# Performance work log

Hardware: AMD Instinct MI355X
Metric: run time of the kernel (lower is better)

The kernel has to match this reference:

```python
import jax, jax.numpy as jnp
import numpy as np

BS, L, D, H, NL, ITEM_NUM = 128, 64, 512, 8, 2, 100000
NEG_INF = -10000.0


def _ln(x):
    m = jnp.mean(x, axis=-1, keepdims=True)
    v = jnp.var(x, axis=-1, keepdims=True)
    return (x - m) * jax.lax.rsqrt(v + 1e-5)


def _user_encoder(input_embs, log_mask, pos_emb, qkv_w, out_w, ffn_w1, ffn_w2):
    # SASRec-style causal transformer encoder (post-LN blocks)
    B, S, d = input_embs.shape
    dh = d // H
    x = _ln(input_embs + pos_emb[None, :, :])
    pad = (log_mask != 0)                                  # [B,S]
    causal = jnp.tril(jnp.ones((S, S), dtype=bool))
    attn_ok = causal[None, :, :] & pad[:, None, :]         # [B,S,S]
    bias = jnp.where(attn_ok, 0.0, NEG_INF)[:, None, :, :]  # [B,1,S,S]
    for l in range(NL):
        qkv = x @ qkv_w[l]                                 # [B,S,3d]
        q, k, v = jnp.split(qkv, 3, axis=-1)
        q = q.reshape(B, S, H, dh).transpose(0, 2, 1, 3)
        k = k.reshape(B, S, H, dh).transpose(0, 2, 1, 3)
        v = v.reshape(B, S, H, dh).transpose(0, 2, 1, 3)
        scores = jnp.einsum('bhqd,bhkd->bhqk', q, k) / jnp.sqrt(jnp.asarray(dh, x.dtype)) + bias
        attn = jax.nn.softmax(scores, axis=-1)
        o = jnp.einsum('bhqk,bhkd->bhqd', attn, v).transpose(0, 2, 1, 3).reshape(B, S, d)
        x = _ln(x + o @ out_w[l])
        h = jax.nn.gelu(x @ ffn_w1[l])
        x = _ln(x + h @ ffn_w2[l])
    return x


def setup_inputs() -> dict:
    key = jax.random.key(0)
    ks = jax.random.split(key, 9)
    sample_items_id = jax.random.randint(ks[0], (BS, L + 1), 0, ITEM_NUM + 1)
    log_mask = jax.random.randint(ks[1], (BS, L), 0, 2).astype(jnp.float32)
    emb_table = (jax.random.normal(ks[2], (ITEM_NUM + 1, D), jnp.float32) * 0.02).at[0].set(0.0)
    pos_emb = jax.random.normal(ks[3], (L, D), jnp.float32) * 0.02
    qkv_w = jax.random.normal(ks[4], (NL, D, 3 * D), jnp.float32) * (D ** -0.5)
    out_w = jax.random.normal(ks[5], (NL, D, D), jnp.float32) * (D ** -0.5)
    ffn_w1 = jax.random.normal(ks[6], (NL, D, 4 * D), jnp.float32) * (D ** -0.5)
    ffn_w2 = jax.random.normal(ks[7], (NL, 4 * D, D), jnp.float32) * ((4 * D) ** -0.5)
    pop_prob = jax.random.uniform(ks[8], (ITEM_NUM + 1,), jnp.float32, 1e-6, 1.0)
    return dict(sample_items_id=sample_items_id, log_mask=log_mask, emb_table=emb_table,
                pos_emb=pos_emb, qkv_w=qkv_w, out_w=out_w, ffn_w1=ffn_w1, ffn_w2=ffn_w2,
                pop_prob=pop_prob)


def reference(sample_items_id, log_mask, emb_table, pos_emb, qkv_w, out_w, ffn_w1, ffn_w2, pop_prob):
    bs, l = log_mask.shape
    N = bs * (l + 1)
    items_flat = sample_items_id.reshape(-1)                        # [N]
    debias = jnp.log(pop_prob[items_flat])                          # [N]
    score_embs = emb_table[items_flat]                              # [N, D]
    input_embs = score_embs.reshape(bs, l + 1, -1)
    prec = _user_encoder(input_embs[:, :-1, :], log_mask, pos_emb, qkv_w, out_w, ffn_w1, ffn_w2)
    prec = prec.reshape(bs * l, -1)                                 # [bs*L, D]
    logits = prec @ score_embs.T - debias[None, :]                  # [bs*L, N]
    # padding-column mask (concat(log_mask, ones) == 0)
    pad_cols = jnp.concatenate([log_mask, jnp.ones((bs, 1), log_mask.dtype)], axis=1).reshape(-1) == 0
    logits = jnp.where(pad_cols[None, :], NEG_INF, logits)
    logits = logits.reshape(bs, l, N)
    # in-batch dedup mask: column k masked for batch i if item k appears in batch i's items
    id_list = sample_items_id.reshape(bs, l + 1)
    member = (items_flat[None, :, None] == id_list[:, None, :]).any(-1)   # [bs, N]
    target_col = jnp.arange(bs)[:, None] * (l + 1) + jnp.arange(1, l + 1)[None, :]  # [bs, L]
    is_target = jnp.arange(N)[None, None, :] == target_col[:, :, None]    # [bs, L, N]
    dedup = member[:, None, :] & ~is_target
    logits = jnp.where(dedup, NEG_INF, logits).reshape(bs * l, N)
    labels = target_col.reshape(-1)                                 # [bs*L]
    logp = jax.nn.log_softmax(logits, axis=-1)
    nll = -jnp.take_along_axis(logp, labels[:, None], axis=1)[:, 0]
    valid = (log_mask.reshape(-1) != 0).astype(logits.dtype)
    return (nll * valid).sum() / valid.sum()
```

## Files before the change

kernel.cpp:

```cpp
#include <hip/hip_runtime.h>
#include <hip/hip_bf16.h>
#include <cstdint>
#include <cstddef>

#define NEG_INF -10000.0f

constexpr int BSZ  = 128;
constexpr int SEQ  = 64;
constexpr int DIM  = 512;
constexpr int HEADS = 8;
constexpr int NLAYER = 2;
constexpr int NCOL = BSZ * (SEQ + 1);
constexpr int NCOLP = 8448;
constexpr int NROW = BSZ * SEQ;
constexpr int NSTRIP = NCOLP / 64;
constexpr float CMAX = 40.0f;
constexpr float LOG2E = 1.4426950408889634f;

typedef __attribute__((ext_vector_type(8))) short bf16x8;
typedef __attribute__((ext_vector_type(4))) float f32x4;

__device__ __forceinline__ void async_copy16(const void* g, void* l) {
    __builtin_amdgcn_global_load_lds(
        (const __attribute__((address_space(1))) void*)g,
        (__attribute__((address_space(3))) void*)l, 16, 0, 0);
}

__device__ __forceinline__ float b2f(uint16_t u) {
    return __builtin_bit_cast(float, (uint32_t)u << 16);
}
__device__ __forceinline__ uint16_t f2b(float f) {
    __hip_bfloat16 h = __float2bfloat16(f);
    return __builtin_bit_cast(uint16_t, h);
}

__device__ __forceinline__ float fexp2(float x) {
    float r; asm("v_exp_f32 %0, %1" : "=v"(r) : "v"(x)); return r;
}

__device__ __forceinline__ float gelu_f(float v) {
    float u = 0.7978845608028654f * (v + 0.044715f * v * v * v);
    float t2 = fexp2(u * (2.0f * LOG2E));
    float th = 1.0f - 2.0f * __builtin_amdgcn_rcpf(t2 + 1.0f);
    return 0.5f * v * (1.0f + th);
}

__device__ __forceinline__ void swizzle_rc(int id, int& ry, int& cx) {
    ry = (id & 7) * 8 + ((id >> 3) & 7);
    cx = id >> 6;
}

#define BAR() __builtin_amdgcn_s_barrier()
#define LGKM0() asm volatile("s_waitcnt lgkmcnt(0)" ::: "memory")
#define VMCNT(n) asm volatile("s_waitcnt vmcnt(" #n ")" ::: "memory")

__global__ __launch_bounds__(256) void gather_posln_kernel(
    const int* __restrict__ ids, const float* __restrict__ table,
    const float* __restrict__ pop, const float* __restrict__ pos,
    __hip_bfloat16* __restrict__ sebf, float* __restrict__ debias,
    float* __restrict__ deb2, __hip_bfloat16* __restrict__ xb) {
    const int w = threadIdx.x >> 6, lane = threadIdx.x & 63;
    const int k = blockIdx.x * 4 + w;
    const int b = k / 65, s = k - b * 65;
    const int id = ids[k];
    const float* src = table + (size_t)id * DIM + lane * 8;
    float4 u0 = *(const float4*)src;
    float4 u1 = *(const float4*)(src + 4);
    float v[8] = {u0.x, u0.y, u0.z, u0.w, u1.x, u1.y, u1.z, u1.w};
    bf16x8 se;
    #pragma unroll
    for (int j = 0; j < 8; j++) se[j] = (short)f2b(v[j]);
    *(bf16x8*)((uint16_t*)sebf + (size_t)k * DIM + lane * 8) = se;
    if (lane == 0) {
        const float lp = logf(pop[id]);
        debias[k] = lp;
        deb2[k] = (lp + CMAX) * LOG2E;
    }
    if (s < 64) {
        const float* pp = pos + (size_t)s * DIM + lane * 8;
        float4 p0 = *(const float4*)pp;
        float4 p1 = *(const float4*)(pp + 4);
        float t[8] = {v[0] + p0.x, v[1] + p0.y, v[2] + p0.z, v[3] + p0.w,
                      v[4] + p1.x, v[5] + p1.y, v[6] + p1.z, v[7] + p1.w};
        float sum = 0.f, sq = 0.f;
        #pragma unroll
        for (int j = 0; j < 8; j++) { sum += t[j]; sq += t[j] * t[j]; }
        #pragma unroll
        for (int off = 32; off > 0; off >>= 1) {
            sum += __shfl_xor(sum, off, 64);
            sq  += __shfl_xor(sq,  off, 64);
        }
        const float mean = sum * (1.0f / 512.0f);
        const float var  = sq * (1.0f / 512.0f) - mean * mean;
        const float rs = rsqrtf(var + 1e-5f);
        bf16x8 o;
        #pragma unroll
        for (int j = 0; j < 8; j++) o[j] = (short)f2b((t[j] - mean) * rs);
        *(bf16x8*)((uint16_t*)xb + (size_t)(b * 64 + s) * DIM + lane * 8) = o;
    }
}

__global__ __launch_bounds__(256) void mask_kernel(
    const int* __restrict__ ids, const float* __restrict__ log_mask,
    uint8_t* __restrict__ colmask, uint8_t* __restrict__ padcol) {
    const int bi = blockIdx.x >> 3, seg = blockIdx.x & 7;
    __shared__ int sid[65];
    if (threadIdx.x < 65) sid[threadIdx.x] = ids[bi * 65 + threadIdx.x];
    __syncthreads();
    const int kend = (seg + 1) * (NCOLP / 8);
    for (int k = seg * (NCOLP / 8) + threadIdx.x; k < kend; k += 256) {
        uint8_t cmv, pcv;
        if (k < NCOL) {
            const int id = ids[k];
            bool mem = false;
            #pragma unroll
            for (int j = 0; j < 65; j++) mem |= (sid[j] == id);
            const int i2 = k / 65, jj = k - i2 * 65;
            const bool pc = (jj < 64) && (log_mask[i2 * 64 + jj] == 0.0f);
            cmv = (mem || pc) ? 1 : 0;
            pcv = pc ? 1 : 0;
        } else { cmv = 1; pcv = 1; }
        colmask[(size_t)bi * NCOLP + k] = cmv;
        if (bi == 0) padcol[k] = pcv;
    }
}

__global__ __launch_bounds__(256) void transpose_bf16_kernel(
    const float* __restrict__ W, __hip_bfloat16* __restrict__ WT, int K, int N) {
    __shared__ float tile[32][33];
    const size_t loff = (size_t)blockIdx.z * K * N;
    const int nt = blockIdx.x * 32, kt = blockIdx.y * 32;
    const int c = threadIdx.x & 31, r = threadIdx.x >> 5;
    #pragma unroll
    for (int p = 0; p < 4; p++)
        tile[p * 8 + r][c] = W[loff + (size_t)(kt + p * 8 + r) * N + nt + c];
    __syncthreads();
    #pragma unroll
    for (int p = 0; p < 4; p++)
        WT[loff + (size_t)(nt + p * 8 + r) * K + kt + c] = __float2bfloat16(tile[c][p * 8 + r]);
}

template<bool SCALED>
__global__ __launch_bounds__(256) void resid_ln_kernel(
    __hip_bfloat16* __restrict__ xb, const __hip_bfloat16* __restrict__ y,
    __hip_bfloat16* __restrict__ xs) {
    const int w = threadIdx.x >> 6, lane = threadIdx.x & 63;
    const int row = blockIdx.x * 4 + w;
    uint16_t* xp = (uint16_t*)xb + (size_t)row * DIM + lane * 8;
    const uint16_t* yp = (const uint16_t*)y + (size_t)row * DIM + lane * 8;
    bf16x8 xv = *(const bf16x8*)xp;
    bf16x8 yv = *(const bf16x8*)yp;
    float t[8];
    float sum = 0.f, sq = 0.f;
    #pragma unroll
    for (int j = 0; j < 8; j++) {
        t[j] = b2f((uint16_t)xv[j]) + b2f((uint16_t)yv[j]);
        sum += t[j]; sq += t[j] * t[j];
    }
    #pragma unroll
    for (int off = 32; off > 0; off >>= 1) {
        sum += __shfl_xor(sum, off, 64);
        sq  += __shfl_xor(sq,  off, 64);
    }
    const float mean = sum * (1.0f / 512.0f);
    const float var  = sq * (1.0f / 512.0f) - mean * mean;
    const float rs = rsqrtf(var + 1e-5f);
    bf16x8 o;
    #pragma unroll
    for (int j = 0; j < 8; j++) o[j] = (short)f2b((t[j] - mean) * rs);
    *(bf16x8*)xp = o;
    if (SCALED) {
        bf16x8 os;
        #pragma unroll
        for (int j = 0; j < 8; j++) os[j] = (short)f2b((t[j] - mean) * rs * LOG2E);
        *(bf16x8*)((uint16_t*)xs + (size_t)row * DIM + lane * 8) = os;
    }
}

template<int TN, bool GELU>
__global__ __launch_bounds__(256) void gemm_bt_kernel(
    const __hip_bfloat16* __restrict__ A, const __hip_bfloat16* __restrict__ Bt,
    __hip_bfloat16* __restrict__ C, int N, int K) {
    __shared__ uint16_t As[2][128][32];
    __shared__ uint16_t Bs[2][TN][32];
    const int tid = threadIdx.x, w = tid >> 6, lane = tid & 63;
    const int quad = lane >> 4, l15 = lane & 15;
    constexpr int AI = (TN == 128) ? 4 : 2;
    const int wr = (TN == 128) ? (w >> 1) : w;
    const int wc = (TN == 128) ? (w & 1) : 0;
    const int rowbase = wr * (AI * 16);
    int ry, cx;
    swizzle_rc(blockIdx.x, ry, cx);
    const int row0 = ry * 128, col0 = cx * TN;
    const uint16_t* Ag = (const uint16_t*)A;
    const uint16_t* Bg = (const uint16_t*)Bt;
    const int sr = lane >> 2, sc = (lane & 3) * 8;
    f32x4 acc[AI][4];
    #pragma unroll
    for (int i = 0; i < AI; i++)
        #pragma unroll
        for (int j = 0; j < 4; j++) acc[i][j] = {0.f, 0.f, 0.f, 0.f};

    for (int k0 = 0; k0 < K; k0 += 64) {
        #pragma unroll
        for (int h = 0; h < 2; h++) {
            #pragma unroll
            for (int i = 0; i < 2; i++) {
                const int rb = w * 32 + i * 16;
                async_copy16(Ag + (size_t)(row0 + rb + sr) * K + k0 + h * 32 + sc, &As[h][rb][0]);
            }
            if (TN == 128) {
                #pragma unroll
                for (int i = 0; i < 2; i++) {
                    const int rb = w * 32 + i * 16;
                    async_copy16(Bg + (size_t)(col0 + rb + sr) * K + k0 + h * 32 + sc, &Bs[h][rb][0]);
                }
            } else {
                const int rb = w * 16;
                async_copy16(Bg + (size_t)(col0 + rb + sr) * K + k0 + h * 32 + sc, &Bs[h][rb][0]);
            }
        }
        __syncthreads();
        #pragma unroll
        for (int h = 0; h < 2; h++) {
            bf16x8 af[AI], bfr[4];
            #pragma unroll
            for (int i = 0; i < AI; i++)
                af[i] = *(const bf16x8*)&As[h][rowbase + i * 16 + l15][quad * 8];
            #pragma unroll
            for (int j = 0; j < 4; j++)
                bfr[j] = *(const bf16x8*)&Bs[h][wc * 64 + j * 16 + l15][quad * 8];
            #pragma unroll
            for (int i = 0; i < AI; i++)
                #pragma unroll
                for (int j = 0; j < 4; j++)
                    acc[i][j] = __builtin_amdgcn_mfma_f32_16x16x32_bf16(af[i], bfr[j], acc[i][j], 0, 0, 0);
        }
        __syncthreads();
    }
    #pragma unroll
    for (int i = 0; i < AI; i++) {
        #pragma unroll
        for (int r = 0; r < 4; r++) {
            const int row = row0 + rowbase + i * 16 + quad * 4 + r;
            #pragma unroll
            for (int j = 0; j < 4; j++) {
                const int col = col0 + wc * 64 + j * 16 + l15;
                float v = acc[i][j][r];
                if (GELU) v = gelu_f(v);
                C[(size_t)row * N + col] = __float2bfloat16(v);
            }
        }
    }
}

__global__ __launch_bounds__(256) void attn_mfma_kernel(
    const __hip_bfloat16* __restrict__ qkv, const float* __restrict__ log_mask,
    __hip_bfloat16* __restrict__ obuf) {
    constexpr int QS = 72;
    constexpr int VS32 = 36;
    __shared__ uint16_t Qs[64 * QS];
    __shared__ uint16_t Ks_[64 * QS];
    __shared__ uint16_t Ps[64 * QS];
    __shared__ uint32_t Vt32[64 * VS32];
    __shared__ float mask_s[64];
    const int b = blockIdx.x >> 3, h = blockIdx.x & 7;
    const int tid = threadIdx.x, w = tid >> 6, lane = tid & 63;
    const int quad = lane >> 4, l15 = lane & 15;
    const uint16_t* qg = (const uint16_t*)qkv;

    if (tid < 64) mask_s[tid] = log_mask[b * 64 + tid];
    #pragma unroll
    for (int it = 0; it < 2; it++) {
        const int idx = it * 256 + tid;
        const int s = idx >> 3, c = (idx & 7) * 8;
        const size_t gbase = (size_t)(b * 64 + s) * 1536 + h * 64 + c;
        *(bf16x8*)&Qs[s * QS + c]  = *(const bf16x8*)&qg[gbase];
        *(bf16x8*)&Ks_[s * QS + c] = *(const bf16x8*)&qg[gbase + 512];
    }
    {
        const int sp = tid >> 3;
        const int c = (tid & 7) * 8;
        const size_t gbase = (size_t)(b * 64 + sp * 2) * 1536 + 1024 + h * 64 + c;
        bf16x8 v0 = *(const bf16x8*)&qg[gbase];
        bf16x8 v1 = *(const bf16x8*)&qg[gbase + 1536];
        #pragma unroll
        for (int jj = 0; jj < 8; jj++)
            Vt32[(c + jj) * VS32 + sp] =
                (uint32_t)(uint16_t)v0[jj] | ((uint32_t)(uint16_t)v1[jj] << 16);
    }
    __syncthreads();

    f32x4 sacc[4];
    #pragma unroll
    for (int j = 0; j < 4; j++) sacc[j] = {0.f, 0.f, 0.f, 0.f};
    #pragma unroll
    for (int k0 = 0; k0 < 2; k0++) {
        bf16x8 aq = *(const bf16x8*)&Qs[(w * 16 + l15) * QS + k0 * 32 + quad * 8];
        #pragma unroll
        for (int j = 0; j < 4; j++) {
            bf16x8 bk = *(const bf16x8*)&Ks_[(j * 16 + l15) * QS + k0 * 32 + quad * 8];
            sacc[j] = __builtin_amdgcn_mfma_f32_16x16x32_bf16(aq, bk, sacc[j], 0, 0, 0);
        }
    }
    #pragma unroll
    for (int r = 0; r < 4; r++) {
        const int q = w * 16 + quad * 4 + r;
        float vals[4];
        float vmax = -3.0e38f;
        #pragma unroll
        for (int j = 0; j < 4; j++) {
            const int col = j * 16 + l15;
            const bool ok = (col <= q) && (mask_s[col] != 0.0f);
            float v = sacc[j][r] * 0.125f + (ok ? 0.0f : NEG_INF);
            vals[j] = v;
            vmax = fmaxf(vmax, v);
        }
        #pragma unroll
        for (int off = 1; off < 16; off <<= 1) vmax = fmaxf(vmax, __shfl_xor(vmax, off, 64));
        float e[4], s = 0.f;
        #pragma unroll
        for (int j = 0; j < 4; j++) { e[j] = fexp2((vals[j] - vmax) * LOG2E); s += e[j]; }
        #pragma unroll
        for (int off = 1; off < 16; off <<= 1) s += __shfl_xor(s, off, 64);
        const float inv = 1.0f / s;
        #pragma unroll
        for (int j = 0; j < 4; j++)
            Ps[q * QS + j * 16 + l15] = f2b(e[j] * inv);
    }
    __syncthreads();

    f32x4 oacc[4];
    #pragma unroll
    for (int j = 0; j < 4; j++) oacc[j] = {0.f, 0.f, 0.f, 0.f};
    #pragma unroll
    for (int k0 = 0; k0 < 2; k0++) {
        bf16x8 ap = *(const bf16x8*)&Ps[(w * 16 + l15) * QS + k0 * 32 + quad * 8];
        #pragma unroll
        for (int j = 0; j < 4; j++) {
            bf16x8 bv = *(const bf16x8*)&Vt32[(j * 16 + l15) * VS32 + k0 * 16 + quad * 4];
            oacc[j] = __builtin_amdgcn_mfma_f32_16x16x32_bf16(ap, bv, oacc[j], 0, 0, 0);
        }
    }
    #pragma unroll
    for (int r = 0; r < 4; r++) {
        const int q = w * 16 + quad * 4 + r;
        #pragma unroll
        for (int j = 0; j < 4; j++) {
            const int d = j * 16 + l15;
            obuf[(size_t)(b * 64 + q) * 512 + h * 64 + d] = __float2bfloat16(oacc[j][r]);
        }
    }
}

__global__ __launch_bounds__(512) void gemm256_logits_kernel(
    const __hip_bfloat16* __restrict__ A, const __hip_bfloat16* __restrict__ Bt,
    int N, int K,
    const float* __restrict__ deb2, const uint8_t* __restrict__ colmask,
    float* __restrict__ partials) {
    __shared__ uint16_t SA[2][2][128 * 64];
    __shared__ uint16_t SB[2][2][128 * 64];
    __shared__ float dc_s[256];
    __shared__ uint8_t cm_s[4][256];

    const int tid = threadIdx.x;
    const int w = tid >> 6, lane = tid & 63;
    const int quad = lane >> 4, l15 = lane & 15;
    const int wr = w >> 2, wc = w & 3;

    const int nwg = gridDim.x;
    const int xid = (blockIdx.x & 7) * (nwg >> 3) + (blockIdx.x >> 3);
    const int ry = xid & 31, cx = xid >> 5;
    const int row0 = ry * 256, col0 = cx * 256;

    const uint16_t* Ag = (const uint16_t*)A;
    const uint16_t* Bg = (const uint16_t*)Bt;

    if (tid < 256) dc_s[tid] = deb2[col0 + tid];
    #pragma unroll
    for (int j = 0; j < 2; j++) {
        const int e = j * 512 + tid;
        cm_s[e >> 8][e & 255] =
            colmask[(size_t)((row0 >> 6) + (e >> 8)) * NCOLP + col0 + (e & 255)];
    }

    const int tb0 = w << 6, tb1 = 512 + (w << 6);
    const uint16_t* gA[2][2];
    const uint16_t* gB[2][2];
    #pragma unroll
    for (int j = 0; j < 2; j++) {
        const int t = j * 512 + (w << 6) + lane;
        const int r = t >> 3;
        const int s = (t & 7) ^ (r & 7);
        #pragma unroll
        for (int h = 0; h < 2; h++) {
            gA[h][j] = Ag + (size_t)(row0 + h * 128 + r) * K + s * 8;
            gB[h][j] = Bg + (size_t)(col0 + h * 128 + r) * K + s * 8;
        }
    }

    #define STAGE_A(tile, half, k0) do { \
        async_copy16(gA[half][0] + (k0), &SA[tile][half][tb0 * 8]); \
        async_copy16(gA[half][1] + (k0), &SA[tile][half][tb1 * 8]); } while (0)
    #define STAGE_B(tile, half, k0) do { \
        async_copy16(gB[half][0] + (k0), &SB[tile][half][tb0 * 8]); \
        async_copy16(gB[half][1] + (k0), &SB[tile][half][tb1 * 8]); } while (0)

    auto fragA = [&](int tile, int m, int kk) -> bf16x8 {
        return *(const bf16x8*)&SA[tile][wr]
            [((m * 16 + l15) << 6) + ((((kk << 2) + quad) ^ (l15 & 7)) << 3)];
    };
    auto fragB = [&](int tile, int n, int kk) -> bf16x8 {
        return *(const bf16x8*)&SB[tile][wc >> 1]
            [(((wc & 1) * 64 + n * 16 + l15) << 6) + ((((kk << 2) + quad) ^ (l15 & 7)) << 3)];
    };

    f32x4 acc[8][4];
    #pragma unroll
    for (int m = 0; m < 8; m++)
        #pragma unroll
        for (int n = 0; n < 4; n++) acc[m][n] = {0.f, 0.f, 0.f, 0.f};

    STAGE_A(0, 0, 0); STAGE_A(0, 1, 0);
    STAGE_B(0, 0, 0); STAGE_B(0, 1, 0);
    STAGE_A(1, 0, 64); STAGE_B(1, 0, 64);
    VMCNT(4);
    BAR();

    const int niters = K >> 7;
    bf16x8 af[4][2], bA[2][2], bB[2][2];
    for (int it = 0; it < niters; ++it) {
        const bool st = (it + 1 < niters);
        const int kc = it << 7;
        const int kn = kc + 128;

        #pragma unroll
        for (int m = 0; m < 4; m++) { af[m][0] = fragA(0, m, 0); af[m][1] = fragA(0, m, 1); }
        #pragma unroll
        for (int n = 0; n < 2; n++) { bA[n][0] = fragB(0, n, 0); bA[n][1] = fragB(0, n, 1); }
        STAGE_A(1, 1, kc + 64);
        BAR(); LGKM0();
        __builtin_amdgcn_s_setprio(1);
        #pragma unroll
        for (int m = 0; m < 4; m++)
            #pragma unroll
            for (int n = 0; n < 2; n++) {
                acc[m][n] = __builtin_amdgcn_mfma_f32_16x16x32_bf16(af[m][0], bA[n][0], acc[m][n], 0, 0, 0);
                acc[m][n] = __builtin_amdgcn_mfma_f32_16x16x32_bf16(af[m][1], bA[n][1], acc[m][n], 0, 0, 0);
            }
        __builtin_amdgcn_s_setprio(0);
        BAR();

        #pragma unroll
        for (int n = 0; n < 2; n++) { bB[n][0] = fragB(0, n + 2, 0); bB[n][1] = fragB(0, n + 2, 1); }
        STAGE_B(1, 1, kc + 64);
        BAR(); LGKM0();
        __builtin_amdgcn_s_setprio(1);
        #pragma unroll
        for (int m = 0; m < 4; m++)
            #pragma unroll
            for (int n = 0; n < 2; n++) {
                acc[m][n + 2] = __builtin_amdgcn_mfma_f32_16x16x32_bf16(af[m][0], bB[n][0], acc[m][n + 2], 0, 0, 0);
                acc[m][n + 2] = __builtin_amdgcn_mfma_f32_16x16x32_bf16(af[m][1], bB[n][1], acc[m][n + 2], 0, 0, 0);
            }
        __builtin_amdgcn_s_setprio(0);
        BAR();

        #pragma unroll
        for (int m = 0; m < 4; m++) { af[m][0] = fragA(0, m + 4, 0); af[m][1] = fragA(0, m + 4, 1); }
        if (st) STAGE_B(0, 0, kn);
        BAR(); LGKM0();
        __builtin_amdgcn_s_setprio(1);
        #pragma unroll
        for (int m = 0; m < 4; m++)
            #pragma unroll
            for (int n = 0; n < 2; n++) {
                acc[m + 4][n + 2] = __builtin_amdgcn_mfma_f32_16x16x32_bf16(af[m][0], bB[n][0], acc[m + 4][n + 2], 0, 0, 0);
                acc[m + 4][n + 2] = __builtin_amdgcn_mfma_f32_16x16x32_bf16(af[m][1], bB[n][1], acc[m + 4][n + 2], 0, 0, 0);
            }
        __builtin_amdgcn_s_setprio(0);
        BAR();

        if (st) STAGE_A(0, 0, kn);
        __builtin_amdgcn_s_setprio(1);
        #pragma unroll
        for (int m = 0; m < 4; m++)
            #pragma unroll
            for (int n = 0; n < 2; n++) {
                acc[m + 4][n] = __builtin_amdgcn_mfma_f32_16x16x32_bf16(af[m][0], bA[n][0], acc[m + 4][n], 0, 0, 0);
                acc[m + 4][n] = __builtin_amdgcn_mfma_f32_16x16x32_bf16(af[m][1], bA[n][1], acc[m + 4][n], 0, 0, 0);
            }
        __builtin_amdgcn_s_setprio(0);
        if (st) { VMCNT(4); } else { VMCNT(0); }
        BAR();

        #pragma unroll
        for (int m = 0; m < 4; m++) { af[m][0] = fragA(1, m, 0); af[m][1] = fragA(1, m, 1); }
        #pragma unroll
        for (int n = 0; n < 2; n++) { bA[n][0] = fragB(1, n, 0); bA[n][1] = fragB(1, n, 1); }
        if (st) STAGE_A(0, 1, kn);
        BAR(); LGKM0();
        __builtin_amdgcn_s_setprio(1);
        #pragma unroll
        for (int m = 0; m < 4; m++)
            #pragma unroll
            for (int n = 0; n < 2; n++) {
                acc[m][n] = __builtin_amdgcn_mfma_f32_16x16x32_bf16(af[m][0], bA[n][0], acc[m][n], 0, 0, 0);
                acc[m][n] = __builtin_amdgcn_mfma_f32_16x16x32_bf16(af[m][1], bA[n][1], acc[m][n], 0, 0, 0);
            }
        __builtin_amdgcn_s_setprio(0);
        BAR();

        #pragma unroll
        for (int n = 0; n < 2; n++) { bB[n][0] = fragB(1, n + 2, 0); bB[n][1] = fragB(1, n + 2, 1); }
        if (st) STAGE_B(0, 1, kn);
        BAR(); LGKM0();
        __builtin_amdgcn_s_setprio(1);
        #pragma unroll
        for (int m = 0; m < 4; m++)
            #pragma unroll
            for (int n = 0; n < 2; n++) {
                acc[m][n + 2] = __builtin_amdgcn_mfma_f32_16x16x32_bf16(af[m][0], bB[n][0], acc[m][n + 2], 0, 0, 0);
                acc[m][n + 2] = __builtin_amdgcn_mfma_f32_16x16x32_bf16(af[m][1], bB[n][1], acc[m][n + 2], 0, 0, 0);
            }
        __builtin_amdgcn_s_setprio(0);
        BAR();

        #pragma unroll
        for (int m = 0; m < 4; m++) { af[m][0] = fragA(1, m + 4, 0); af[m][1] = fragA(1, m + 4, 1); }
        if (st) STAGE_B(1, 0, kn + 64);
        BAR(); LGKM0();
        __builtin_amdgcn_s_setprio(1);
        #pragma unroll
        for (int m = 0; m < 4; m++)
            #pragma unroll
            for (int n = 0; n < 2; n++) {
                acc[m + 4][n + 2] = __builtin_amdgcn_mfma_f32_16x16x32_bf16(af[m][0], bB[n][0], acc[m + 4][n + 2], 0, 0, 0);
                acc[m + 4][n + 2] = __builtin_amdgcn_mfma_f32_16x16x32_bf16(af[m][1], bB[n][1], acc[m + 4][n + 2], 0, 0, 0);
            }
        __builtin_amdgcn_s_setprio(0);
        BAR();

        if (st) STAGE_A(1, 0, kn + 64);
        __builtin_amdgcn_s_setprio(1);
        #pragma unroll
        for (int m = 0; m < 4; m++)
            #pragma unroll
            for (int n = 0; n < 2; n++) {
                acc[m + 4][n] = __builtin_amdgcn_mfma_f32_16x16x32_bf16(af[m][0], bA[n][0], acc[m + 4][n], 0, 0, 0);
                acc[m + 4][n] = __builtin_amdgcn_mfma_f32_16x16x32_bf16(af[m][1], bA[n][1], acc[m + 4][n], 0, 0, 0);
            }
        __builtin_amdgcn_s_setprio(0);
        if (st) { VMCNT(4); BAR(); }
    }

    {
        const int strip = cx * 4 + wc;
        #pragma unroll
        for (int m = 0; m < 8; m++) {
            #pragma unroll
            for (int r = 0; r < 4; r++) {
                const int lrow = wr * 128 + m * 16 + quad * 4 + r;
                const int row = row0 + lrow;
                float s = 0.f;
                #pragma unroll
                for (int n = 0; n < 4; n++) {
                    const int lcol = wc * 64 + n * 16 + l15;
                    float t = acc[m][n][r] - dc_s[lcol];
                    t = (cm_s[lrow >> 6][lcol] != 0) ? -1.0e30f : t;
                    s += fexp2(t);
                }
                #pragma unroll
                for (int off = 1; off < 16; off <<= 1) s += __shfl_xor(s, off, 64);
                if (l15 == 0) partials[(size_t)row * NSTRIP + strip] = s;
            }
        }
    }
    #undef STAGE_A
    #undef STAGE_B
}

__global__ __launch_bounds__(256) void label_kernel(
    const __hip_bfloat16* __restrict__ xb, const __hip_bfloat16* __restrict__ sebf,
    const float* __restrict__ debias, const uint8_t* __restrict__ padcol,
    float* __restrict__ lab) {
    const int w = threadIdx.x >> 6, lane = threadIdx.x & 63;
    const int row = blockIdx.x * 4 + w;
    const int b = row >> 6, s0 = row & 63;
    const int k = b * 65 + s0 + 1;
    const uint16_t* xp = (const uint16_t*)xb + (size_t)row * DIM + lane * 8;
    const uint16_t* sp = (const uint16_t*)sebf + (size_t)k * DIM + lane * 8;
    bf16x8 xv = *(const bf16x8*)xp;
    bf16x8 sv = *(const bf16x8*)sp;
    float a = 0.f;
    #pragma unroll
    for (int j = 0; j < 8; j++) a += b2f((uint16_t)xv[j]) * b2f((uint16_t)sv[j]);
    #pragma unroll
    for (int off = 32; off > 0; off >>= 1) a += __shfl_xor(a, off, 64);
    if (lane == 0)
        lab[row] = padcol[k] ? NEG_INF : (a - debias[k]);
}

__global__ __launch_bounds__(256) void combine_kernel(
    const float* __restrict__ partials, const float* __restrict__ label_logit,
    const float* __restrict__ log_mask, float* __restrict__ bsums) {
    const int row = blockIdx.x * 256 + threadIdx.x;
    const float lab = label_logit[row];
    float Ls = fexp2((lab - CMAX) * LOG2E);
    const float4* pr = (const float4*)(partials + (size_t)row * NSTRIP);
    for (int t = 0; t < NSTRIP / 4; t++) {
        float4 v = pr[t];
        Ls += v.x + v.y + v.z + v.w;
    }
    const float lse = CMAX + logf(Ls);
    const float valid = (log_mask[row] != 0.0f) ? 1.0f : 0.0f;
    float a = (lse - lab) * valid;
    float c = valid;
    __shared__ float sa[4], sc_[4];
    #pragma unroll
    for (int off = 32; off > 0; off >>= 1) {
        a += __shfl_down(a, off, 64);
        c += __shfl_down(c, off, 64);
    }
    const int lane = threadIdx.x & 63, w = threadIdx.x >> 6;
    if (lane == 0) { sa[w] = a; sc_[w] = c; }
    __syncthreads();
    if (threadIdx.x == 0) {
        bsums[blockIdx.x * 2 + 0] = sa[0] + sa[1] + sa[2] + sa[3];
        bsums[blockIdx.x * 2 + 1] = sc_[0] + sc_[1] + sc_[2] + sc_[3];
    }
}

__global__ __launch_bounds__(64) void finalize_kernel(
    const float* __restrict__ bsums, float* __restrict__ out) {
    const int t = threadIdx.x;
    float a = 0.f, c = 0.f;
    if (t < 32) { a = bsums[2 * t]; c = bsums[2 * t + 1]; }
    #pragma unroll
    for (int off = 32; off > 0; off >>= 1) {
        a += __shfl_down(a, off, 64);
        c += __shfl_down(c, off, 64);
    }
    if (t == 0) out[0] = a / c;
}

extern "C" void kernel_launch(void* const* d_in, const int* in_sizes, int n_in,
                              void* d_out, int out_size, void* d_ws, size_t ws_size,
                              hipStream_t stream) {
    const int*   ids    = (const int*)d_in[0];
    const float* lm     = (const float*)d_in[1];
    const float* emb    = (const float*)d_in[2];
    const float* pos    = (const float*)d_in[3];
    const float* qkv_w  = (const float*)d_in[4];
    const float* out_w  = (const float*)d_in[5];
    const float* ffn1_w = (const float*)d_in[6];
    const float* ffn2_w = (const float*)d_in[7];
    const float* pop    = (const float*)d_in[8];
    float* out = (float*)d_out;

    char* p = (char*)d_ws;
    auto alloc = [&](size_t bytes) {
        char* r = p;
        p += (bytes + 255) & ~(size_t)255;
        return r;
    };
    typedef __hip_bfloat16 bf16;
    bf16*    sebf     = (bf16*)alloc((size_t)NCOLP * DIM * 2);
    float*   debias   = (float*)alloc((size_t)NCOLP * 4);
    float*   deb2     = (float*)alloc((size_t)NCOLP * 4);
    uint8_t* padcol   = (uint8_t*)alloc(NCOLP);
    uint8_t* colmask  = (uint8_t*)alloc((size_t)BSZ * NCOLP);
    bf16*    xb       = (bf16*)alloc((size_t)NROW * DIM * 2);
    bf16*    xbs      = (bf16*)alloc((size_t)NROW * DIM * 2);
    bf16*    big      = (bf16*)alloc((size_t)NROW * 2048 * 2);
    bf16*    tmp1     = (bf16*)alloc((size_t)NROW * DIM * 2);
    bf16*    tmp2     = (bf16*)alloc((size_t)NROW * DIM * 2);
    float*   partials = (float*)alloc((size_t)NROW * NSTRIP * 4);
    float*   lab      = (float*)alloc((size_t)NROW * 4);
    float*   bsums    = (float*)alloc(64 * 4);
    bf16*    qkvT     = (bf16*)alloc((size_t)NLAYER * 1536 * 512 * 2);
    bf16*    outT     = (bf16*)alloc((size_t)NLAYER * 512 * 512 * 2);
    bf16*    f1T      = (bf16*)alloc((size_t)NLAYER * 2048 * 512 * 2);
    bf16*    f2T      = (bf16*)alloc((size_t)NLAYER * 512 * 2048 * 2);

    transpose_bf16_kernel<<<dim3(1536 / 32, 512 / 32, NLAYER), 256, 0, stream>>>(
        qkv_w, qkvT, 512, 1536);
    transpose_bf16_kernel<<<dim3(512 / 32, 512 / 32, NLAYER), 256, 0, stream>>>(
        out_w, outT, 512, 512);
    transpose_bf16_kernel<<<dim3(2048 / 32, 512 / 32, NLAYER), 256, 0, stream>>>(
        ffn1_w, f1T, 512, 2048);
    transpose_bf16_kernel<<<dim3(512 / 32, 2048 / 32, NLAYER), 256, 0, stream>>>(
        ffn2_w, f2T, 2048, 512);

    gather_posln_kernel<<<NCOL / 4, 256, 0, stream>>>(ids, emb, pop, pos, sebf, debias, deb2, xb);
    mask_kernel<<<BSZ * 8, 256, 0, stream>>>(ids, lm, colmask, padcol);

    for (int l = 0; l < NLAYER; l++) {
        gemm_bt_kernel<128, false><<<(1536 / 128) * 64, 256, 0, stream>>>(
            xb, qkvT + (size_t)l * 1536 * 512, big, 1536, 512);
        attn_mfma_kernel<<<BSZ * HEADS, 256, 0, stream>>>(big, lm, tmp1);
        gemm_bt_kernel<64, false><<<(512 / 64) * 64, 256, 0, stream>>>(
            tmp1, outT + (size_t)l * 512 * 512, tmp2, 512, 512);
        resid_ln_kernel<false><<<NROW / 4, 256, 0, stream>>>(xb, tmp2, nullptr);
        gemm_bt_kernel<128, true><<<(2048 / 128) * 64, 256, 0, stream>>>(
            xb, f1T + (size_t)l * 2048 * 512, big, 2048, 512);
        gemm_bt_kernel<64, false><<<(512 / 64) * 64, 256, 0, stream>>>(
            big, f2T + (size_t)l * 512 * 2048, tmp2, 512, 2048);
        if (l == NLAYER - 1)
            resid_ln_kernel<true><<<NROW / 4, 256, 0, stream>>>(xb, tmp2, xbs);
        else
            resid_ln_kernel<false><<<NROW / 4, 256, 0, stream>>>(xb, tmp2, nullptr);
    }

    label_kernel<<<NROW / 4, 256, 0, stream>>>(xb, sebf, debias, padcol, lab);
    gemm256_logits_kernel<<<32 * (NCOLP / 256), 512, 0, stream>>>(
        xbs, sebf, NCOLP, 512, deb2, colmask, partials);
    combine_kernel<<<NROW / 256, 256, 0, stream>>>(partials, lab, lm, bsums);
    finalize_kernel<<<1, 64, 0, stream>>>(bsums, out);
}
```

Before: 628.1 us.

## Pipeline encoder GEMM loads with double-buffered async copies and swizzled LDS

```diff
diff --git a/kernel.cpp b/kernel.cpp
--- a/kernel.cpp
+++ b/kernel.cpp
@@ -178,14 +178,14 @@
 }
 
 template<int TN, bool GELU>
-__global__ __launch_bounds__(256) void gemm_bt_kernel(
+__global__ __launch_bounds__(256) void gemm_bt2_kernel(
     const __hip_bfloat16* __restrict__ A, const __hip_bfloat16* __restrict__ Bt,
     __hip_bfloat16* __restrict__ C, int N, int K) {
-    __shared__ uint16_t As[2][128][32];
-    __shared__ uint16_t Bs[2][TN][32];
+    constexpr int AI = (TN == 128) ? 4 : 2;
+    __shared__ uint16_t As[2][128 * 32];
+    __shared__ uint16_t Bs[2][TN * 32];
     const int tid = threadIdx.x, w = tid >> 6, lane = tid & 63;
     const int quad = lane >> 4, l15 = lane & 15;
-    constexpr int AI = (TN == 128) ? 4 : 2;
     const int wr = (TN == 128) ? (w >> 1) : w;
     const int wc = (TN == 128) ? (w & 1) : 0;
     const int rowbase = wr * (AI * 16);
@@ -194,50 +194,58 @@
     const int row0 = ry * 128, col0 = cx * TN;
     const uint16_t* Ag = (const uint16_t*)A;
     const uint16_t* Bg = (const uint16_t*)Bt;
-    const int sr = lane >> 2, sc = (lane & 3) * 8;
+
+    const int srow = lane >> 2;
+    const int ssl = ((lane & 3) ^ ((lane >> 3) & 3)) * 8;
+    const uint16_t* sA0 = Ag + (size_t)(row0 + w * 16 + srow) * K + ssl;
+    const uint16_t* sA1 = sA0 + (size_t)64 * K;
+    const uint16_t* sB0 = Bg + (size_t)(col0 + w * 16 + srow) * K + ssl;
+    const uint16_t* sB1 = sB0 + (size_t)64 * K;
+
+    auto STAGE = [&](int buf, int kk) {
+        async_copy16(sA0 + kk, &As[buf][w * 512]);
+        async_copy16(sA1 + kk, &As[buf][2048 + w * 512]);
+        async_copy16(sB0 + kk, &Bs[buf][w * 512]);
+        if (TN == 128) async_copy16(sB1 + kk, &Bs[buf][2048 + w * 512]);
+    };
+
     f32x4 acc[AI][4];
     #pragma unroll
     for (int i = 0; i < AI; i++)
         #pragma unroll
         for (int j = 0; j < 4; j++) acc[i][j] = {0.f, 0.f, 0.f, 0.f};
 
-    for (int k0 = 0; k0 < K; k0 += 64) {
-        #pragma unroll
-        for (int h = 0; h < 2; h++) {
-            #pragma unroll
-            for (int i = 0; i < 2; i++) {
-                const int rb = w * 32 + i * 16;
-                async_copy16(Ag + (size_t)(row0 + rb + sr) * K + k0 + h * 32 + sc, &As[h][rb][0]);
-            }
-            if (TN == 128) {
-                #pragma unroll
-                for (int i = 0; i < 2; i++) {
-                    const int rb = w * 32 + i * 16;
-                    async_copy16(Bg + (size_t)(col0 + rb + sr) * K + k0 + h * 32 + sc, &Bs[h][rb][0]);
-                }
-            } else {
-                const int rb = w * 16;
-                async_copy16(Bg + (size_t)(col0 + rb + sr) * K + k0 + h * 32 + sc, &Bs[h][rb][0]);
-            }
-        }
-        __syncthreads();
-        #pragma unroll
-        for (int h = 0; h < 2; h++) {
-            bf16x8 af[AI], bfr[4];
-            #pragma unroll
-            for (int i = 0; i < AI; i++)
-                af[i] = *(const bf16x8*)&As[h][rowbase + i * 16 + l15][quad * 8];
+    STAGE(0, 0); STAGE(1, 32);
+    if (TN == 128) { VMCNT(4); } else { VMCNT(3); }
+    BAR();
+
+    const int NT = K >> 5;
+    const int swz = (quad ^ ((l15 >> 1) & 3)) * 8;
+    for (int t = 0; t < NT; ++t) {
+        const int buf = t & 1;
+        bf16x8 af[AI], bfr[4];
+        #pragma unroll
+        for (int i = 0; i < AI; i++)
+            af[i] = *(const bf16x8*)&As[buf][(rowbase + i * 16 + l15) * 32 + swz];
+        #pragma unroll
+        for (int j = 0; j < 4; j++)
+            bfr[j] = *(const bf16x8*)&Bs[buf][(wc * 64 + j * 16 + l15) * 32 + swz];
+        LGKM0();
+        __builtin_amdgcn_sched_barrier(0);
+        BAR();
+        if (t + 2 < NT) STAGE(buf, (t + 2) * 32);
+        __builtin_amdgcn_s_setprio(1);
+        #pragma unroll
+        for (int i = 0; i < AI; i++)
             #pragma unroll
             for (int j = 0; j < 4; j++)
-                bfr[j] = *(const bf16x8*)&Bs[h][wc * 64 + j * 16 + l15][quad * 8];
-            #pragma unroll
-            for (int i = 0; i < AI; i++)
-                #pragma unroll
-                for (int j = 0; j < 4; j++)
-                    acc[i][j] = __builtin_amdgcn_mfma_f32_16x16x32_bf16(af[i], bfr[j], acc[i][j], 0, 0, 0);
-        }
-        __syncthreads();
-    }
+                acc[i][j] = __builtin_amdgcn_mfma_f32_16x16x32_bf16(af[i], bfr[j], acc[i][j], 0, 0, 0);
+        __builtin_amdgcn_s_setprio(0);
+        if (t + 2 < NT) { if (TN == 128) { VMCNT(4); } else { VMCNT(3); } }
+        else if (t + 1 < NT) { VMCNT(0); }
+        BAR();
+    }
+
     #pragma unroll
     for (int i = 0; i < AI; i++) {
         #pragma unroll
@@ -696,15 +704,15 @@
     mask_kernel<<<BSZ * 8, 256, 0, stream>>>(ids, lm, colmask, padcol);
 
     for (int l = 0; l < NLAYER; l++) {
-        gemm_bt_kernel<128, false><<<(1536 / 128) * 64, 256, 0, stream>>>(
+        gemm_bt2_kernel<128, false><<<(1536 / 128) * 64, 256, 0, stream>>>(
             xb, qkvT + (size_t)l * 1536 * 512, big, 1536, 512);
         attn_mfma_kernel<<<BSZ * HEADS, 256, 0, stream>>>(big, lm, tmp1);
-        gemm_bt_kernel<64, false><<<(512 / 64) * 64, 256, 0, stream>>>(
+        gemm_bt2_kernel<64, false><<<(512 / 64) * 64, 256, 0, stream>>>(
             tmp1, outT + (size_t)l * 512 * 512, tmp2, 512, 512);
         resid_ln_kernel<false><<<NROW / 4, 256, 0, stream>>>(xb, tmp2, nullptr);
-        gemm_bt_kernel<128, true><<<(2048 / 128) * 64, 256, 0, stream>>>(
+        gemm_bt2_kernel<128, true><<<(2048 / 128) * 64, 256, 0, stream>>>(
             xb, f1T + (size_t)l * 2048 * 512, big, 2048, 512);
-        gemm_bt_kernel<64, false><<<(512 / 64) * 64, 256, 0, stream>>>(
+        gemm_bt2_kernel<64, false><<<(512 / 64) * 64, 256, 0, stream>>>(
             big, f2T + (size_t)l * 512 * 2048, tmp2, 512, 2048);
         if (l == NLAYER - 1)
             resid_ln_kernel<true><<<NROW / 4, 256, 0, stream>>>(xb, tmp2, xbs);
```

Result: no change. 625.6 us (-0.4%).
